# Performance work log

Hardware: AMD Instinct MI355X
Metric: run time of the kernel (lower is better)

Reference implementation:

```python
import jax, jax.numpy as jnp
import numpy as np

D = 1024
H = 16
HD = D // H
DFF = 4 * D
LN_EPS = 1e-5

def layernorm(x, gamma, beta):
    mu = jnp.mean(x, axis=-1, keepdims=True)
    var = jnp.mean(jnp.square(x - mu), axis=-1, keepdims=True)
    return (x - mu) * jax.lax.rsqrt(var + LN_EPS) * gamma + beta

def setup_inputs() -> dict:
    key = jax.random.key(0)
    ks = jax.random.split(key, 10)
    B, Nq, Nk = 2, 2048, 2048
    s = 0.02
    return {
        "q_x": jax.random.normal(ks[0], (B, Nq, D), jnp.float32),
        "kv_x": jax.random.normal(ks[1], (B, Nk, D), jnp.float32),
        "Wq": jax.random.normal(ks[2], (D, D), jnp.float32) * s,
        "Wkv": jax.random.normal(ks[3], (2 * D, D), jnp.float32) * s,
        "Wo": jax.random.normal(ks[4], (D, D), jnp.float32) * s,
        "bo": jnp.zeros((D,), jnp.float32),
        "ln_q_g": jnp.ones((D,), jnp.float32),
        "ln_q_b": jnp.zeros((D,), jnp.float32),
        "ln_kv_g": jnp.ones((D,), jnp.float32),
        "ln_kv_b": jnp.zeros((D,), jnp.float32),
        "W1": jax.random.normal(ks[5], (DFF, D), jnp.float32) * s,
        "b1": jnp.zeros((DFF,), jnp.float32),
        "W2": jax.random.normal(ks[6], (D, DFF), jnp.float32) * s,
        "b2": jnp.zeros((D,), jnp.float32),
    }

def reference(q_x, kv_x, Wq, Wkv, Wo, bo, ln_q_g, ln_q_b, ln_kv_g, ln_kv_b, W1, b1, W2, b2):
    B, Nq, _ = q_x.shape
    Nk = kv_x.shape[1]
    scale = HD ** -0.5
    # norm + projections
    q = layernorm(q_x, ln_q_g, ln_q_b) @ Wq.T                    # [B,Nq,D]
    kv = layernorm(kv_x, ln_kv_g, ln_kv_b) @ Wkv.T               # [B,Nk,2D]
    q = q.reshape(B, Nq, H, HD).transpose(0, 2, 1, 3)            # [B,H,Nq,hd]
    kv = kv.reshape(B, Nk, 2, H, HD).transpose(2, 0, 3, 1, 4)    # [2,B,H,Nk,hd]
    k, v = kv[0], kv[1]
    attn = jnp.einsum('bhqd,bhkd->bhqk', q, k) * scale           # [B,H,Nq,Nk]
    attn = jax.nn.softmax(attn, axis=-1)
    out = jnp.einsum('bhqk,bhkd->bhqd', attn, v)
    out = out.transpose(0, 2, 1, 3).reshape(B, Nq, D)
    x = q_x + out @ Wo.T + bo
    h = jax.nn.silu(x @ W1.T + b1)
    x = x + h @ W2.T + b2
    return x
```

## Files before the change

kernel.cpp:

```cpp
#include <hip/hip_runtime.h>

using u16   = unsigned short;
using f32x4 = __attribute__((ext_vector_type(4))) float;
using s16x8 = __attribute__((ext_vector_type(8))) short;
using u32x2 = __attribute__((ext_vector_type(2))) unsigned int;
using u32x4 = __attribute__((ext_vector_type(4))) unsigned int;

#define LOG2E 1.44269504088896f

static __device__ __forceinline__ u16 f2bf(float f) {
  union { float f; unsigned u; } a; a.f = f;
  unsigned r = a.u + 0x7fffu + ((a.u >> 16) & 1u);
  return (u16)(r >> 16);
}
static __device__ __forceinline__ unsigned cvtpk(float lo, float hi) {
  unsigned r;
  asm("v_cvt_pk_bf16_f32 %0, %1, %2" : "=v"(r) : "v"(lo), "v"(hi));
  return r;
}

static __device__ __forceinline__ void gload16(const void* g, void* l) {
  __builtin_amdgcn_global_load_lds(
      (__attribute__((address_space(1))) unsigned int*)g,
      (__attribute__((address_space(3))) unsigned int*)l, 16, 0, 0);
}

__global__ __launch_bounds__(256) void ln2_k(
    const float* __restrict__ xq, const float* __restrict__ xk,
    const float* __restrict__ gq, const float* __restrict__ bq,
    const float* __restrict__ gk, const float* __restrict__ bk,
    u16* __restrict__ oq, u16* __restrict__ ok)
{
  int row = blockIdx.x;
  const float* x; const float* gam; const float* bet; u16* out;
  if (row < 4096) { x = xq; gam = gq; bet = bq; out = oq; }
  else { row -= 4096; x = xk; gam = gk; bet = bk; out = ok; }
  const int t = threadIdx.x;
  const float4 v = ((const float4*)(x + (size_t)row * 1024))[t];
  float s  = v.x + v.y + v.z + v.w;
  float ss = v.x*v.x + v.y*v.y + v.z*v.z + v.w*v.w;
  #pragma unroll
  for (int m = 1; m < 64; m <<= 1) { s += __shfl_xor(s, m); ss += __shfl_xor(ss, m); }
  __shared__ float red[8];
  const int w = t >> 6;
  if ((t & 63) == 0) { red[w] = s; red[4 + w] = ss; }
  __syncthreads();
  s  = red[0] + red[1] + red[2] + red[3];
  ss = red[4] + red[5] + red[6] + red[7];
  const float mu   = s * (1.0f / 1024.0f);
  const float rstd = rsqrtf(ss * (1.0f / 1024.0f) - mu * mu + 1e-5f);
  const float4 gv = ((const float4*)gam)[t];
  const float4 bv = ((const float4*)bet)[t];
  ushort4 o;
  o.x = f2bf((v.x - mu) * rstd * gv.x + bv.x);
  o.y = f2bf((v.y - mu) * rstd * gv.y + bv.y);
  o.z = f2bf((v.z - mu) * rstd * gv.z + bv.z);
  o.w = f2bf((v.w - mu) * rstd * gv.w + bv.w);
  ((ushort4*)(out + (size_t)row * 1024))[t] = o;
}

__global__ __launch_bounds__(256) void cast_all_k(
    const float* __restrict__ Wq, const float* __restrict__ Wkv,
    const float* __restrict__ Wo, const float* __restrict__ W1,
    const float* __restrict__ W2,
    u16* __restrict__ wq_b, u16* __restrict__ wkv_b, u16* __restrict__ wo_b,
    u16* __restrict__ w1_b, u16* __restrict__ w2_b)
{
  const int i = blockIdx.x * 256 + threadIdx.x;
  const float* src; u16* dst; int off; float sc = 1.0f;
  if      (i <  262144) { src = Wq;  dst = wq_b;  off = i; sc = 0.125f; }
  else if (i <  786432) { src = Wkv; dst = wkv_b; off = i -  262144; }
  else if (i < 1048576) { src = Wo;  dst = wo_b;  off = i -  786432; }
  else if (i < 2097152) { src = W1;  dst = w1_b;  off = i - 1048576; }
  else                  { src = W2;  dst = w2_b;  off = i - 2097152; }
  const float4 v = ((const float4*)src)[off];
  ushort4 o;
  o.x = f2bf(v.x * sc); o.y = f2bf(v.y * sc); o.z = f2bf(v.z * sc); o.w = f2bf(v.w * sc);
  ((ushort4*)dst)[off] = o;
}

template<int BIAS, int RES, int SILU, int OF32, int OBF>
static __device__ __forceinline__ void gemm_body(
    const u16* __restrict__ A, const u16* __restrict__ B,
    u16* __restrict__ Cb, float* __restrict__ Cf,
    const float* __restrict__ bias, const float* __restrict__ resid,
    int N, int K, int bid, u16* smem)
{
  const int tid = threadIdx.x;
  const int w = tid >> 6, l = tid & 63;
  const int g = l >> 4, q = l & 15;
  const int ntn = N >> 7;
  const int bm = bid / ntn, bn = bid - bm * ntn;
  const int wr = w >> 1, wc = w & 1;
  const int sw = (q & 7) << 4;
  f32x4 acc[2][4] = {};

  const size_t abase = (size_t)(bm * 128) * K;
  const size_t bbase = (size_t)(bn * 128) * K;

  auto stage = [&](int buf, int k0) {
    u16* as = smem + buf * 8192;
    u16* bs = smem + 16384 + buf * 8192;
    #pragma unroll
    for (int r = 0; r < 2; ++r) {
      const int c = (r << 9) + tid;
      const int row = c >> 3, part = c & 7;
      const int sp = part ^ (row & 7);
      gload16(A + abase + (size_t)row * K + k0 + sp * 8,
              as + (size_t)((r << 9) + (w << 6)) * 8);
      gload16(B + bbase + (size_t)row * K + k0 + sp * 8,
              bs + (size_t)((r << 9) + (w << 6)) * 8);
    }
  };

  const int NT = K >> 6;
  stage(0, 0);
  asm volatile("s_waitcnt vmcnt(0)" ::: "memory");
  __syncthreads();
  int cur = 0;
  for (int t = 0; t < NT; ++t) {
    if (t + 1 < NT) stage(cur ^ 1, (t + 1) << 6);
    const char* as = (const char*)(smem + cur * 8192);
    const char* bs = (const char*)(smem + 16384 + cur * 8192);
    #pragma unroll
    for (int ks = 0; ks < 2; ++ks) {
      s16x8 af[2], bfr[4];
      #pragma unroll
      for (int m = 0; m < 2; ++m)
        af[m] = *(const s16x8*)(as + (size_t)(wr * 32 + m * 16 + q) * 128 +
                                ((ks * 64 + g * 16) ^ sw));
      #pragma unroll
      for (int n = 0; n < 4; ++n)
        bfr[n] = *(const s16x8*)(bs + (size_t)(wc * 64 + n * 16 + q) * 128 +
                                 ((ks * 64 + g * 16) ^ sw));
      #pragma unroll
      for (int m = 0; m < 2; ++m)
        #pragma unroll
        for (int n = 0; n < 4; ++n)
          acc[m][n] = __builtin_amdgcn_mfma_f32_16x16x32_bf16(af[m], bfr[n], acc[m][n], 0, 0, 0);
    }
    asm volatile("s_waitcnt vmcnt(0)" ::: "memory");
    __syncthreads();
    cur ^= 1;
  }

  #pragma unroll
  for (int m = 0; m < 2; ++m) {
    const int row0 = bm * 128 + wr * 32 + m * 16 + g * 4;
    #pragma unroll
    for (int n = 0; n < 4; ++n) {
      const int col = bn * 128 + wc * 64 + n * 16 + q;
      float bv = 0.0f;
      if (BIAS) bv = bias[col];
      #pragma unroll
      for (int r = 0; r < 4; ++r) {
        const size_t idx = (size_t)(row0 + r) * N + col;
        float v = acc[m][n][r] + bv;
        if (RES)  v += resid[idx];
        if (SILU) v = v / (1.0f + __expf(-v));
        if (OF32) Cf[idx] = v;
        if (OBF)  Cb[idx] = f2bf(v);
      }
    }
  }
}

template<int BIAS, int RES, int SILU, int OF32, int OBF>
__global__ __launch_bounds__(512, 4) void gemm_k(
    const u16* __restrict__ A, const u16* __restrict__ B,
    u16* __restrict__ Cb, float* __restrict__ Cf,
    const float* __restrict__ bias, const float* __restrict__ resid,
    int N, int K)
{
  __shared__ u16 smem[32768];
  gemm_body<BIAS, RES, SILU, OF32, OBF>(A, B, Cb, Cf, bias, resid, N, K, blockIdx.x, smem);
}

__global__ __launch_bounds__(512, 4) void gemm_qkv_k(
    const u16* __restrict__ lnq, const u16* __restrict__ wq, u16* __restrict__ qp,
    const u16* __restrict__ lnk, const u16* __restrict__ wkv, u16* __restrict__ kvp)
{
  __shared__ u16 smem[32768];
  if (blockIdx.x < 256)
    gemm_body<0,0,0,0,1>(lnq, wq, qp, nullptr, nullptr, nullptr, 1024, 1024, blockIdx.x, smem);
  else
    gemm_body<0,0,0,0,1>(lnk, wkv, kvp, nullptr, nullptr, nullptr, 2048, 1024, blockIdx.x - 256, smem);
}

__global__ __launch_bounds__(256, 4) void attn_k(
    const u16* __restrict__ Q, const u16* __restrict__ KV, u16* __restrict__ O)
{
  __shared__ u16 Ks[2][64 * 64];
  __shared__ u16 Vs[2][64 * 64];
  __shared__ u16 Ps[4][16 * 64];
  const int tid = threadIdx.x;
  const int w = tid >> 6, l = tid & 63;
  const int g = l >> 4, q = l & 15;
  const int bh = blockIdx.x >> 5, qt = blockIdx.x & 31;
  const int b = bh >> 4, h = bh & 15;
  const int sw = (q & 7) << 4;

  const size_t qrow = (size_t)(b * 2048 + qt * 64 + w * 16 + q);
  s16x8 qf[2];
  qf[0] = *(const s16x8*)&Q[qrow * 1024 + h * 64 + g * 8];
  qf[1] = *(const s16x8*)&Q[qrow * 1024 + h * 64 + 32 + g * 8];

  f32x4 oacc[4] = {};
  float mrow = -1e30f, lrow = 0.0f;

  const u16* kvb = KV + (size_t)b * 2048 * 2048;
  const unsigned vs_base =
      (unsigned)(unsigned long long)(__attribute__((address_space(3))) u16*)Vs;
  char* pb = (char*)Ps + w * 2048;

  auto stage = [&](int buf, int kv0) {
    #pragma unroll
    for (int r = 0; r < 2; ++r) {
      const int c = (r << 8) + tid;
      const int krow = c >> 3, slot = c & 7;
      gload16(kvb + (size_t)(kv0 + krow) * 2048 + h * 64 + ((slot ^ (krow & 7)) << 3),
              &Ks[buf][(size_t)((r << 8) + (w << 6)) * 8]);
      const int vkv = ((c >> 3) & 15) * 4 + ((c >> 1) & 3);
      const int vd0 = ((c >> 7) & 3) * 16 + (c & 1) * 8;
      gload16(kvb + (size_t)(kv0 + vkv) * 2048 + 1024 + h * 64 + vd0,
              &Vs[buf][(size_t)((r << 8) + (w << 6)) * 8]);
    }
  };

  stage(0, 0);
  asm volatile("s_waitcnt vmcnt(0)" ::: "memory");
  __syncthreads();
  int cur = 0;

  for (int kt = 0; kt < 32; ++kt) {
    if (kt + 1 < 32) stage(cur ^ 1, (kt + 1) * 64);

    const char* ksb = (const char*)Ks[cur];
    f32x4 sacc[4] = {};
    #pragma unroll
    for (int s = 0; s < 2; ++s)
      #pragma unroll
      for (int nf = 0; nf < 4; ++nf) {
        const int krw = nf * 16 + q;
        const s16x8 kf = *(const s16x8*)(ksb + krw * 128 +
                              ((s * 64 + g * 16) ^ ((krw & 7) << 4)));
        sacc[nf] = __builtin_amdgcn_mfma_f32_16x16x32_bf16(kf, qf[s], sacc[nf], 0, 0, 0);
      }

    float mx = sacc[0][0];
    #pragma unroll
    for (int nf = 0; nf < 4; ++nf)
      #pragma unroll
      for (int r = 0; r < 4; ++r) mx = fmaxf(mx, sacc[nf][r]);
    mx = fmaxf(mx, __shfl_xor(mx, 16));
    mx = fmaxf(mx, __shfl_xor(mx, 32));
    if (__any(mx > mrow + 8.0f)) {
      const float mnew = fmaxf(mrow, mx);
      const float al = __builtin_amdgcn_exp2f((mrow - mnew) * LOG2E);
      lrow *= al;
      float ar[4];
      #pragma unroll
      for (int r = 0; r < 4; ++r) ar[r] = __shfl(al, g * 4 + r);
      #pragma unroll
      for (int nf = 0; nf < 4; ++nf)
        #pragma unroll
        for (int r = 0; r < 4; ++r) oacc[nf][r] *= ar[r];
      mrow = mnew;
    }
    float rs = 0.0f;
    #pragma unroll
    for (int nf = 0; nf < 4; ++nf)
      #pragma unroll
      for (int r = 0; r < 4; ++r) {
        const float e = __builtin_amdgcn_exp2f((sacc[nf][r] - mrow) * LOG2E);
        sacc[nf][r] = e; rs += e;
      }
    rs += __shfl_xor(rs, 16);
    rs += __shfl_xor(rs, 32);
    lrow += rs;

    #pragma unroll
    for (int nf = 0; nf < 4; ++nf) {
      const unsigned w0 = cvtpk(sacc[nf][0], sacc[nf][1]);
      const unsigned w1 = cvtpk(sacc[nf][2], sacc[nf][3]);
      *(unsigned*)(pb + q * 128 + ((32 * nf + 8 * g    ) ^ sw)) = w0;
      *(unsigned*)(pb + q * 128 + ((32 * nf + 8 * g + 4) ^ sw)) = w1;
    }

    const unsigned vsb = vs_base + (unsigned)(cur << 13);
    #pragma unroll
    for (int s = 0; s < 2; ++s) {
      const int o1 = s * 64 + g * 8;
      const u32x2 pa  = *(const u32x2*)(pb + q * 128 + (o1 ^ sw));
      const u32x2 pb2 = *(const u32x2*)(pb + q * 128 + ((o1 + 32) ^ sw));
      union { u32x4 u; s16x8 s8; } au;
      au.u[0] = pa[0]; au.u[1] = pa[1]; au.u[2] = pb2[0]; au.u[3] = pb2[1];
      #pragma unroll
      for (int nf = 0; nf < 4; ++nf) {
        const unsigned a1 = vsb + (unsigned)((nf * 16 + 8 * s + g) * 128 + 2 * q);
        u32x2 t1, t2;
        asm volatile("ds_read_b64_tr_b16 %0, %2\n\t"
                     "ds_read_b64_tr_b16 %1, %2 offset:512\n\t"
                     "s_waitcnt lgkmcnt(0)"
                     : "=&v"(t1), "=&v"(t2) : "v"(a1) : "memory");
        __builtin_amdgcn_sched_barrier(0);
        union { u32x4 u; s16x8 s8; } bu;
        bu.u[0] = t1[0]; bu.u[1] = t1[1]; bu.u[2] = t2[0]; bu.u[3] = t2[1];
        oacc[nf] = __builtin_amdgcn_mfma_f32_16x16x32_bf16(au.s8, bu.s8, oacc[nf], 0, 0, 0);
      }
    }

    asm volatile("s_waitcnt vmcnt(0)" ::: "memory");
    __syncthreads();
    cur ^= 1;
  }

  float lr[4];
  #pragma unroll
  for (int r = 0; r < 4; ++r) lr[r] = __shfl(lrow, g * 4 + r);
  const size_t ob = (size_t)(b * 2048 + qt * 64 + w * 16) * 1024 + h * 64;
  #pragma unroll
  for (int r = 0; r < 4; ++r) {
    const float inv = 1.0f / lr[r];
    #pragma unroll
    for (int nf = 0; nf < 4; ++nf)
      O[ob + (size_t)(g * 4 + r) * 1024 + nf * 16 + q] = f2bf(oacc[nf][r] * inv);
  }
}

extern "C" void kernel_launch(void* const* d_in, const int* in_sizes, int n_in,
                              void* d_out, int out_size, void* d_ws, size_t ws_size,
                              hipStream_t stream)
{
  const float* q_x  = (const float*)d_in[0];
  const float* kv_x = (const float*)d_in[1];
  const float* Wq   = (const float*)d_in[2];
  const float* Wkv  = (const float*)d_in[3];
  const float* Wo   = (const float*)d_in[4];
  const float* bo   = (const float*)d_in[5];
  const float* lnqg = (const float*)d_in[6];
  const float* lnqb = (const float*)d_in[7];
  const float* lnkg = (const float*)d_in[8];
  const float* lnkb = (const float*)d_in[9];
  const float* W1   = (const float*)d_in[10];
  const float* b1   = (const float*)d_in[11];
  const float* W2   = (const float*)d_in[12];
  const float* b2   = (const float*)d_in[13];
  float* out = (float*)d_out;

  char* ws = (char*)d_ws;
  const size_t MB = 1024 * 1024;
  u16*   wq_b  = (u16*)  (ws +  0 * MB);
  u16*   wkv_b = (u16*)  (ws +  2 * MB);
  u16*   wo_b  = (u16*)  (ws +  6 * MB);
  u16*   w1_b  = (u16*)  (ws +  8 * MB);
  u16*   w2_b  = (u16*)  (ws + 16 * MB);
  u16*   lnq   = (u16*)  (ws + 24 * MB);
  u16*   lnk   = (u16*)  (ws + 32 * MB);
  u16*   qp    = (u16*)  (ws + 40 * MB);
  u16*   kvp   = (u16*)  (ws + 48 * MB);
  u16*   ao    = (u16*)  (ws + 64 * MB);
  float* xf    = (float*)(ws + 72 * MB);
  u16*   xb    = (u16*)  (ws + 88 * MB);
  u16*   hb    = (u16*)  (ws + 96 * MB);

  cast_all_k<<<dim3(12288), dim3(256), 0, stream>>>(
      Wq, Wkv, Wo, W1, W2, wq_b, wkv_b, wo_b, w1_b, w2_b);
  ln2_k<<<dim3(8192), dim3(256), 0, stream>>>(
      q_x, kv_x, lnqg, lnqb, lnkg, lnkb, lnq, lnk);

  gemm_qkv_k<<<dim3(768), dim3(512), 0, stream>>>(lnq, wq_b, qp, lnk, wkv_b, kvp);
  attn_k<<<dim3(1024), dim3(256), 0, stream>>>(qp, kvp, ao);
  gemm_k<1,1,0,1,1><<<dim3(256),  dim3(512), 0, stream>>>(
      ao, wo_b, xb, xf, bo, q_x, 1024, 1024);
  gemm_k<1,0,1,0,1><<<dim3(1024), dim3(512), 0, stream>>>(
      xb, w1_b, hb, nullptr, b1, nullptr, 4096, 1024);
  gemm_k<1,1,0,1,0><<<dim3(256),  dim3(512), 0, stream>>>(
      hb, w2_b, nullptr, out, b2, xf, 1024, 4096);
}
```

Baseline: 236.9 us.

## Keep softmax probabilities in registers, fold log2e into Q scale, fuse prep kernels

Softmax probabilities are packed to bf16 directly into the MFMA A-operand instead of being written to and reread from LDS. The log2(e) factor is folded into the Wq cast scale so exp2 needs no extra multiply. The weight cast and layernorm kernels merge into one launch, and s_setprio raises wave priority around the MFMA loops. Correctness depends on the accumulator layout matching the P operand layout expected by the V MFMA.

```diff
diff --git a/kernel.cpp b/kernel.cpp
--- a/kernel.cpp
+++ b/kernel.cpp
@@ -25,17 +25,36 @@
       (__attribute__((address_space(3))) unsigned int*)l, 16, 0, 0);
 }
 
-__global__ __launch_bounds__(256) void ln2_k(
+__global__ __launch_bounds__(256) void prep_k(
+    const float* __restrict__ Wq, const float* __restrict__ Wkv,
+    const float* __restrict__ Wo, const float* __restrict__ W1,
+    const float* __restrict__ W2,
+    u16* __restrict__ wq_b, u16* __restrict__ wkv_b, u16* __restrict__ wo_b,
+    u16* __restrict__ w1_b, u16* __restrict__ w2_b,
     const float* __restrict__ xq, const float* __restrict__ xk,
     const float* __restrict__ gq, const float* __restrict__ bq,
     const float* __restrict__ gk, const float* __restrict__ bk,
     u16* __restrict__ oq, u16* __restrict__ ok)
 {
-  int row = blockIdx.x;
+  const int blk = blockIdx.x, t = threadIdx.x;
+  if (blk < 12288) {
+    const int i = blk * 256 + t;
+    const float* src; u16* dst; int off; float sc = 1.0f;
+    if      (i <  262144) { src = Wq;  dst = wq_b;  off = i; sc = 0.125f * LOG2E; }
+    else if (i <  786432) { src = Wkv; dst = wkv_b; off = i -  262144; }
+    else if (i < 1048576) { src = Wo;  dst = wo_b;  off = i -  786432; }
+    else if (i < 2097152) { src = W1;  dst = w1_b;  off = i - 1048576; }
+    else                  { src = W2;  dst = w2_b;  off = i - 2097152; }
+    const float4 v = ((const float4*)src)[off];
+    ushort4 o;
+    o.x = f2bf(v.x * sc); o.y = f2bf(v.y * sc); o.z = f2bf(v.z * sc); o.w = f2bf(v.w * sc);
+    ((ushort4*)dst)[off] = o;
+    return;
+  }
+  int row = blk - 12288;
   const float* x; const float* gam; const float* bet; u16* out;
   if (row < 4096) { x = xq; gam = gq; bet = bq; out = oq; }
   else { row -= 4096; x = xk; gam = gk; bet = bk; out = ok; }
-  const int t = threadIdx.x;
   const float4 v = ((const float4*)(x + (size_t)row * 1024))[t];
   float s  = v.x + v.y + v.z + v.w;
   float ss = v.x*v.x + v.y*v.y + v.z*v.z + v.w*v.w;
@@ -59,26 +78,6 @@
   ((ushort4*)(out + (size_t)row * 1024))[t] = o;
 }
 
-__global__ __launch_bounds__(256) void cast_all_k(
-    const float* __restrict__ Wq, const float* __restrict__ Wkv,
-    const float* __restrict__ Wo, const float* __restrict__ W1,
-    const float* __restrict__ W2,
-    u16* __restrict__ wq_b, u16* __restrict__ wkv_b, u16* __restrict__ wo_b,
-    u16* __restrict__ w1_b, u16* __restrict__ w2_b)
-{
-  const int i = blockIdx.x * 256 + threadIdx.x;
-  const float* src; u16* dst; int off; float sc = 1.0f;
-  if      (i <  262144) { src = Wq;  dst = wq_b;  off = i; sc = 0.125f; }
-  else if (i <  786432) { src = Wkv; dst = wkv_b; off = i -  262144; }
-  else if (i < 1048576) { src = Wo;  dst = wo_b;  off = i -  786432; }
-  else if (i < 2097152) { src = W1;  dst = w1_b;  off = i - 1048576; }
-  else                  { src = W2;  dst = w2_b;  off = i - 2097152; }
-  const float4 v = ((const float4*)src)[off];
-  ushort4 o;
-  o.x = f2bf(v.x * sc); o.y = f2bf(v.y * sc); o.z = f2bf(v.z * sc); o.w = f2bf(v.w * sc);
-  ((ushort4*)dst)[off] = o;
-}
-
 template<int BIAS, int RES, int SILU, int OF32, int OBF>
 static __device__ __forceinline__ void gemm_body(
     const u16* __restrict__ A, const u16* __restrict__ B,
@@ -192,13 +191,11 @@
 {
   __shared__ u16 Ks[2][64 * 64];
   __shared__ u16 Vs[2][64 * 64];
-  __shared__ u16 Ps[4][16 * 64];
   const int tid = threadIdx.x;
   const int w = tid >> 6, l = tid & 63;
   const int g = l >> 4, q = l & 15;
   const int bh = blockIdx.x >> 5, qt = blockIdx.x & 31;
   const int b = bh >> 4, h = bh & 15;
-  const int sw = (q & 7) << 4;
 
   const size_t qrow = (size_t)(b * 2048 + qt * 64 + w * 16 + q);
   s16x8 qf[2];
@@ -211,7 +208,6 @@
   const u16* kvb = KV + (size_t)b * 2048 * 2048;
   const unsigned vs_base =
       (unsigned)(unsigned long long)(__attribute__((address_space(3))) u16*)Vs;
-  char* pb = (char*)Ps + w * 2048;
 
   auto stage = [&](int buf, int kv0) {
     #pragma unroll
@@ -237,6 +233,7 @@
 
     const char* ksb = (const char*)Ks[cur];
     f32x4 sacc[4] = {};
+    __builtin_amdgcn_s_setprio(1);
     #pragma unroll
     for (int s = 0; s < 2; ++s)
       #pragma unroll
@@ -246,6 +243,7 @@
                               ((s * 64 + g * 16) ^ ((krw & 7) << 4)));
         sacc[nf] = __builtin_amdgcn_mfma_f32_16x16x32_bf16(kf, qf[s], sacc[nf], 0, 0, 0);
       }
+    __builtin_amdgcn_s_setprio(0);
 
     float mx = sacc[0][0];
     #pragma unroll
@@ -256,7 +254,7 @@
     mx = fmaxf(mx, __shfl_xor(mx, 32));
     if (__any(mx > mrow + 8.0f)) {
       const float mnew = fmaxf(mrow, mx);
-      const float al = __builtin_amdgcn_exp2f((mrow - mnew) * LOG2E);
+      const float al = __builtin_amdgcn_exp2f(mrow - mnew);
       lrow *= al;
       float ar[4];
       #pragma unroll
@@ -272,29 +270,22 @@
     for (int nf = 0; nf < 4; ++nf)
       #pragma unroll
       for (int r = 0; r < 4; ++r) {
-        const float e = __builtin_amdgcn_exp2f((sacc[nf][r] - mrow) * LOG2E);
+        const float e = __builtin_amdgcn_exp2f(sacc[nf][r] - mrow);
         sacc[nf][r] = e; rs += e;
       }
     rs += __shfl_xor(rs, 16);
     rs += __shfl_xor(rs, 32);
     lrow += rs;
 
-    #pragma unroll
-    for (int nf = 0; nf < 4; ++nf) {
-      const unsigned w0 = cvtpk(sacc[nf][0], sacc[nf][1]);
-      const unsigned w1 = cvtpk(sacc[nf][2], sacc[nf][3]);
-      *(unsigned*)(pb + q * 128 + ((32 * nf + 8 * g    ) ^ sw)) = w0;
-      *(unsigned*)(pb + q * 128 + ((32 * nf + 8 * g + 4) ^ sw)) = w1;
-    }
-
     const unsigned vsb = vs_base + (unsigned)(cur << 13);
+    __builtin_amdgcn_s_setprio(1);
     #pragma unroll
     for (int s = 0; s < 2; ++s) {
-      const int o1 = s * 64 + g * 8;
-      const u32x2 pa  = *(const u32x2*)(pb + q * 128 + (o1 ^ sw));
-      const u32x2 pb2 = *(const u32x2*)(pb + q * 128 + ((o1 + 32) ^ sw));
       union { u32x4 u; s16x8 s8; } au;
-      au.u[0] = pa[0]; au.u[1] = pa[1]; au.u[2] = pb2[0]; au.u[3] = pb2[1];
+      au.u[0] = cvtpk(sacc[2*s  ][0], sacc[2*s  ][1]);
+      au.u[1] = cvtpk(sacc[2*s  ][2], sacc[2*s  ][3]);
+      au.u[2] = cvtpk(sacc[2*s+1][0], sacc[2*s+1][1]);
+      au.u[3] = cvtpk(sacc[2*s+1][2], sacc[2*s+1][3]);
       #pragma unroll
       for (int nf = 0; nf < 4; ++nf) {
         const unsigned a1 = vsb + (unsigned)((nf * 16 + 8 * s + g) * 128 + 2 * q);
@@ -309,6 +300,7 @@
         oacc[nf] = __builtin_amdgcn_mfma_f32_16x16x32_bf16(au.s8, bu.s8, oacc[nf], 0, 0, 0);
       }
     }
+    __builtin_amdgcn_s_setprio(0);
 
     asm volatile("s_waitcnt vmcnt(0)" ::: "memory");
     __syncthreads();
@@ -364,9 +356,8 @@
   u16*   xb    = (u16*)  (ws + 88 * MB);
   u16*   hb    = (u16*)  (ws + 96 * MB);
 
-  cast_all_k<<<dim3(12288), dim3(256), 0, stream>>>(
-      Wq, Wkv, Wo, W1, W2, wq_b, wkv_b, wo_b, w1_b, w2_b);
-  ln2_k<<<dim3(8192), dim3(256), 0, stream>>>(
+  prep_k<<<dim3(20480), dim3(256), 0, stream>>>(
+      Wq, Wkv, Wo, W1, W2, wq_b, wkv_b, wo_b, w1_b, w2_b,
       q_x, kv_x, lnqg, lnqb, lnkg, lnkb, lnq, lnk);
 
   gemm_qkv_k<<<dim3(768), dim3(512), 0, stream>>>(lnq, wq_b, qp, lnk, wkv_b, kvp);
```

Result: faster. 226.8 us (-4.3%).
